# Kernel optimization log

Hardware: AMD Instinct MI355X
Metric: run time of the kernel (lower is better)

Reference implementation:

```python
import jax, jax.numpy as jnp
import numpy as np

M, K, N = 4096, 4096, 4096          # tokens, in_features, out_features
ROW_BLOCK, COL_BLOCK = 1, 4          # sparse block shape (rows x cols of W)
BLOCK_DENSITY = 0.2                  # fraction of nonzero blocks


def setup_inputs() -> dict:
    key = jax.random.key(0)
    k1, k2, k3, k4 = jax.random.split(key, 4)
    # quint8 activations stored as int32 in [0, 255]
    x_q = jax.random.randint(k1, (M, K), 0, 256, dtype=jnp.int32)
    # qint8 weights stored as int32 in [-127, 127], zero_point == 0
    w_dense = jax.random.randint(k2, (N, K), -127, 128, dtype=jnp.int32)
    # block-sparse structure: zero out whole ROW_BLOCK x COL_BLOCK blocks
    blk_mask = jax.random.bernoulli(k3, BLOCK_DENSITY, (N // ROW_BLOCK, K // COL_BLOCK))
    mask = jnp.repeat(jnp.repeat(blk_mask, ROW_BLOCK, axis=0), COL_BLOCK, axis=1)
    w_q = jnp.where(mask, w_dense, 0)
    bias = jax.random.normal(k4, (N,), dtype=jnp.float32) * 0.1
    return dict(
        x_q=x_q,
        w_q=w_q,
        bias=bias,
        x_scale=jnp.float32(0.05),
        x_zp=jnp.int32(128),
        w_scale=jnp.float32(0.01),
        out_scale=jnp.float32(0.1),
        out_zp=jnp.int32(128),
    )


def reference(x_q, w_q, bias, x_scale, x_zp, w_scale, out_scale, out_zp):
    # int32 accumulate of (x - x_zp) @ W^T over the (block-)sparse weight
    acc = jnp.einsum('mk,nk->mn', x_q - x_zp, w_q)  # [M, N] int32
    # dequantize + bias
    y = acc.astype(jnp.float32) * (x_scale * w_scale) + bias[None, :]
    # requantize to quint8 (stored as int32)
    q = jnp.round(y / out_scale).astype(jnp.int32) + out_zp
    return jnp.clip(q, 0, 255)
```

## Files before the change

### kernel.cpp

```cpp
#include <hip/hip_runtime.h>
#include <stdint.h>

#define MDIM 4096
#define NDIM 4096
#define KDIM 4096
#define BM 128
#define BN 128
#define BKB 128

typedef int i32x4 __attribute__((ext_vector_type(4)));

typedef __attribute__((address_space(1))) const void gv_t;
typedef __attribute__((address_space(3))) void lv_t;

__device__ __forceinline__ int pack4(int a, int b, int c, int d) {
    return (a & 0xFF) | ((b & 0xFF) << 8) | ((c & 0xFF) << 16) | ((d & 0xFF) << 24);
}

__global__ void pack_x_kernel(const int* __restrict__ x, const int* __restrict__ zp_p,
                              int* __restrict__ out, int total16) {
    const int zp = zp_p[0];
    int idx = blockIdx.x * blockDim.x + threadIdx.x;
    int stride = gridDim.x * blockDim.x;
    for (int i = idx; i < total16; i += stride) {
        const int4* src = (const int4*)(x + (long)i * 16);
        int4 a = src[0], b = src[1], c = src[2], d = src[3];
        int4 r;
        r.x = pack4(a.x - zp, a.y - zp, a.z - zp, a.w - zp);
        r.y = pack4(b.x - zp, b.y - zp, b.z - zp, b.w - zp);
        r.z = pack4(c.x - zp, c.y - zp, c.z - zp, c.w - zp);
        r.w = pack4(d.x - zp, d.y - zp, d.z - zp, d.w - zp);
        ((int4*)out)[i] = r;
    }
}

__global__ void pack_w_kernel(const int* __restrict__ w, int* __restrict__ out, int total16) {
    int idx = blockIdx.x * blockDim.x + threadIdx.x;
    int stride = gridDim.x * blockDim.x;
    for (int i = idx; i < total16; i += stride) {
        const int4* src = (const int4*)(w + (long)i * 16);
        int4 a = src[0], b = src[1], c = src[2], d = src[3];
        int4 r;
        r.x = pack4(a.x, a.y, a.z, a.w);
        r.y = pack4(b.x, b.y, b.z, b.w);
        r.z = pack4(c.x, c.y, c.z, c.w);
        r.w = pack4(d.x, d.y, d.z, d.w);
        ((int4*)out)[i] = r;
    }
}

__global__ __launch_bounds__(256)
void gemm_i8_kernel(const char* __restrict__ A8, const char* __restrict__ B8,
                    const float* __restrict__ bias,
                    const float* __restrict__ xs_p, const float* __restrict__ ws_p,
                    const float* __restrict__ os_p, const int* __restrict__ ozp_p,
                    int* __restrict__ out) {
    __shared__ char lsA[BM * BKB];
    __shared__ char lsB[BN * BKB];

    const int t = threadIdx.x;
    const int lane = t & 63;
    const int wave = t >> 6;
    const int wr = wave >> 1;
    const int wc = wave & 1;
    const long brow = (long)blockIdx.y * BM;
    const long bcol = (long)blockIdx.x * BN;

    i32x4 acc[4][4] = {};

    int st_row[4], st_off[4];
    #pragma unroll
    for (int i = 0; i < 4; ++i) {
        int c = t + i * 256;
        int r = c >> 3, s = c & 7;
        st_row[i] = r;
        st_off[i] = (s ^ (r & 7)) * 16;
    }

    for (int kt = 0; kt < KDIM; kt += BKB) {
        #pragma unroll
        for (int i = 0; i < 4; ++i) {
            int c16 = (t + i * 256) * 16;
            __builtin_amdgcn_global_load_lds(
                (gv_t*)(A8 + (brow + st_row[i]) * KDIM + kt + st_off[i]),
                (lv_t*)(lsA + c16), 16, 0, 0);
            __builtin_amdgcn_global_load_lds(
                (gv_t*)(B8 + (bcol + st_row[i]) * KDIM + kt + st_off[i]),
                (lv_t*)(lsB + c16), 16, 0, 0);
        }
        __syncthreads();

        i32x4 af[4][2], bf[4][2];
        #pragma unroll
        for (int mi = 0; mi < 4; ++mi) {
            int row = wr * 64 + mi * 16 + (lane & 15);
            #pragma unroll
            for (int kk = 0; kk < 2; ++kk) {
                int ls = kk * 4 + (lane >> 4);
                af[mi][kk] = *(const i32x4*)(lsA + row * BKB + ((ls ^ (row & 7)) * 16));
            }
        }
        #pragma unroll
        for (int ni = 0; ni < 4; ++ni) {
            int row = wc * 64 + ni * 16 + (lane & 15);
            #pragma unroll
            for (int kk = 0; kk < 2; ++kk) {
                int ls = kk * 4 + (lane >> 4);
                bf[ni][kk] = *(const i32x4*)(lsB + row * BKB + ((ls ^ (row & 7)) * 16));
            }
        }

        #pragma unroll
        for (int mi = 0; mi < 4; ++mi)
            #pragma unroll
            for (int ni = 0; ni < 4; ++ni) {
                acc[mi][ni] = __builtin_amdgcn_mfma_i32_16x16x64_i8(af[mi][0], bf[ni][0], acc[mi][ni], 0, 0, 0);
                acc[mi][ni] = __builtin_amdgcn_mfma_i32_16x16x64_i8(af[mi][1], bf[ni][1], acc[mi][ni], 0, 0, 0);
            }
        __syncthreads();
    }

    const float scale = xs_p[0] * ws_p[0];
    const float os = os_p[0];
    const int ozp = ozp_p[0];
    #pragma unroll
    for (int mi = 0; mi < 4; ++mi) {
        long row0 = brow + wr * 64 + mi * 16 + (lane >> 4) * 4;
        #pragma unroll
        for (int ni = 0; ni < 4; ++ni) {
            long col = bcol + wc * 64 + ni * 16 + (lane & 15);
            float bv = bias[col];
            #pragma unroll
            for (int r = 0; r < 4; ++r) {
                float y = (float)acc[mi][ni][r] * scale + bv;
                int q = (int)rintf(y / os) + ozp;
                q = q < 0 ? 0 : (q > 255 ? 255 : q);
                out[(row0 + r) * NDIM + col] = q;
            }
        }
    }
}

__global__ void naive_gemm_kernel(const int* __restrict__ x, const int* __restrict__ w,
                                  const float* __restrict__ bias,
                                  const float* __restrict__ xs_p, const int* __restrict__ xzp_p,
                                  const float* __restrict__ ws_p, const float* __restrict__ os_p,
                                  const int* __restrict__ ozp_p, int* __restrict__ out) {
    long idx = (long)blockIdx.x * blockDim.x + threadIdx.x;
    if (idx >= (long)MDIM * NDIM) return;
    int m = idx >> 12, n = idx & (NDIM - 1);
    const int4* xr = (const int4*)(x + (long)m * KDIM);
    const int4* wv = (const int4*)(w + (long)n * KDIM);
    const int zp = xzp_p[0];
    int acc = 0;
    for (int k = 0; k < KDIM / 4; ++k) {
        int4 a = xr[k], b = wv[k];
        acc += (a.x - zp) * b.x + (a.y - zp) * b.y + (a.z - zp) * b.z + (a.w - zp) * b.w;
    }
    float y = (float)acc * (xs_p[0] * ws_p[0]) + bias[n];
    int q = (int)rintf(y / os_p[0]) + ozp_p[0];
    out[idx] = q < 0 ? 0 : (q > 255 ? 255 : q);
}

extern "C" void kernel_launch(void* const* d_in, const int* in_sizes, int n_in,
                              void* d_out, int out_size, void* d_ws, size_t ws_size,
                              hipStream_t stream) {
    const int*   x_q  = (const int*)d_in[0];
    const int*   w_q  = (const int*)d_in[1];
    const float* bias = (const float*)d_in[2];
    const float* xs   = (const float*)d_in[3];
    const int*   xzp  = (const int*)d_in[4];
    const float* wsc  = (const float*)d_in[5];
    const float* osc  = (const float*)d_in[6];
    const int*   ozp  = (const int*)d_in[7];
    int* out = (int*)d_out;

    const size_t need = 2UL * MDIM * KDIM;
    if (ws_size >= need) {
        char* A8 = (char*)d_ws;
        char* B8 = A8 + (size_t)MDIM * KDIM;
        const int total16 = MDIM * KDIM / 16;
        pack_x_kernel<<<2048, 256, 0, stream>>>(x_q, xzp, (int*)A8, total16);
        pack_w_kernel<<<2048, 256, 0, stream>>>(w_q, (int*)B8, total16);
        dim3 grid(NDIM / BN, MDIM / BM);
        gemm_i8_kernel<<<grid, 256, 0, stream>>>(A8, B8, bias, xs, wsc, osc, ozp, out);
    } else {
        long total = (long)MDIM * NDIM;
        naive_gemm_kernel<<<(total + 255) / 256, 256, 0, stream>>>(
            x_q, w_q, bias, xs, xzp, wsc, osc, ozp, out);
    }
}
```

Baseline: 262.3 us.

## Rewrite int8 GEMM as 256x256 tile, double-buffered, eight-phase pipelined kernel

Grows the GEMM tile to 256x256 with 512 threads. It double-buffers LDS at 128KB and interleaves the global-to-LDS staging of the next tiles with four MFMA sub-phases, using explicit waitcnt, barriers and setprio. It also swizzles the workgroup order for L2 locality and simplifies the pack kernels to one int4 per thread. The aim is to hide global load latency and raise MFMA utilisation, at the cost of heavier register and LDS use, a grid of only 256 workgroups, and more barriers.

```diff
diff --git a/kernel.cpp b/kernel.cpp
--- a/kernel.cpp
+++ b/kernel.cpp
@@ -4,100 +4,100 @@
 #define MDIM 4096
 #define NDIM 4096
 #define KDIM 4096
-#define BM 128
-#define BN 128
+#define BM 256
+#define BN 256
 #define BKB 128
+#define NT (KDIM / BKB)
 
 typedef int i32x4 __attribute__((ext_vector_type(4)));
 
 typedef __attribute__((address_space(1))) const void gv_t;
 typedef __attribute__((address_space(3))) void lv_t;
 
+#define BAR() do { asm volatile("" ::: "memory"); __builtin_amdgcn_s_barrier(); asm volatile("" ::: "memory"); } while (0)
+
 __device__ __forceinline__ int pack4(int a, int b, int c, int d) {
     return (a & 0xFF) | ((b & 0xFF) << 8) | ((c & 0xFF) << 16) | ((d & 0xFF) << 24);
 }
 
 __global__ void pack_x_kernel(const int* __restrict__ x, const int* __restrict__ zp_p,
-                              int* __restrict__ out, int total16) {
+                              int* __restrict__ out, int total4) {
     const int zp = zp_p[0];
-    int idx = blockIdx.x * blockDim.x + threadIdx.x;
-    int stride = gridDim.x * blockDim.x;
-    for (int i = idx; i < total16; i += stride) {
-        const int4* src = (const int4*)(x + (long)i * 16);
-        int4 a = src[0], b = src[1], c = src[2], d = src[3];
-        int4 r;
-        r.x = pack4(a.x - zp, a.y - zp, a.z - zp, a.w - zp);
-        r.y = pack4(b.x - zp, b.y - zp, b.z - zp, b.w - zp);
-        r.z = pack4(c.x - zp, c.y - zp, c.z - zp, c.w - zp);
-        r.w = pack4(d.x - zp, d.y - zp, d.z - zp, d.w - zp);
-        ((int4*)out)[i] = r;
-    }
-}
-
-__global__ void pack_w_kernel(const int* __restrict__ w, int* __restrict__ out, int total16) {
-    int idx = blockIdx.x * blockDim.x + threadIdx.x;
-    int stride = gridDim.x * blockDim.x;
-    for (int i = idx; i < total16; i += stride) {
-        const int4* src = (const int4*)(w + (long)i * 16);
-        int4 a = src[0], b = src[1], c = src[2], d = src[3];
-        int4 r;
-        r.x = pack4(a.x, a.y, a.z, a.w);
-        r.y = pack4(b.x, b.y, b.z, b.w);
-        r.z = pack4(c.x, c.y, c.z, c.w);
-        r.w = pack4(d.x, d.y, d.z, d.w);
-        ((int4*)out)[i] = r;
-    }
-}
-
-__global__ __launch_bounds__(256)
-void gemm_i8_kernel(const char* __restrict__ A8, const char* __restrict__ B8,
-                    const float* __restrict__ bias,
-                    const float* __restrict__ xs_p, const float* __restrict__ ws_p,
-                    const float* __restrict__ os_p, const int* __restrict__ ozp_p,
-                    int* __restrict__ out) {
-    __shared__ char lsA[BM * BKB];
-    __shared__ char lsB[BN * BKB];
+    int i = blockIdx.x * blockDim.x + threadIdx.x;
+    if (i < total4) {
+        int4 a = ((const int4*)x)[i];
+        out[i] = pack4(a.x - zp, a.y - zp, a.z - zp, a.w - zp);
+    }
+}
+
+__global__ void pack_w_kernel(const int* __restrict__ w, int* __restrict__ out, int total4) {
+    int i = blockIdx.x * blockDim.x + threadIdx.x;
+    if (i < total4) {
+        int4 a = ((const int4*)w)[i];
+        out[i] = pack4(a.x, a.y, a.z, a.w);
+    }
+}
+
+__global__ __launch_bounds__(512, 2)
+void gemm_i8_8ph(const char* __restrict__ A8, const char* __restrict__ B8,
+                 const float* __restrict__ bias,
+                 const float* __restrict__ xs_p, const float* __restrict__ ws_p,
+                 const float* __restrict__ os_p, const int* __restrict__ ozp_p,
+                 int* __restrict__ out) {
+    __shared__ char lds[131072];
 
     const int t = threadIdx.x;
     const int lane = t & 63;
     const int wave = t >> 6;
-    const int wr = wave >> 1;
-    const int wc = wave & 1;
-    const long brow = (long)blockIdx.y * BM;
-    const long bcol = (long)blockIdx.x * BN;
-
-    i32x4 acc[4][4] = {};
-
-    int st_row[4], st_off[4];
-    #pragma unroll
-    for (int i = 0; i < 4; ++i) {
-        int c = t + i * 256;
-        int r = c >> 3, s = c & 7;
-        st_row[i] = r;
-        st_off[i] = (s ^ (r & 7)) * 16;
-    }
-
-    for (int kt = 0; kt < KDIM; kt += BKB) {
-        #pragma unroll
-        for (int i = 0; i < 4; ++i) {
-            int c16 = (t + i * 256) * 16;
+    const int wr = wave >> 2;
+    const int wc = wave & 3;
+
+    int wg = blockIdx.x;
+    int swz = (wg & 7) * (256 / 8) + (wg >> 3);
+    const long brow = (long)(swz >> 4) * BM;
+    const long bcol = (long)(swz & 15) * BN;
+
+    i32x4 acc[8][4] = {};
+
+    auto STAGE_HALF = [&](int tt, int h) {
+        if (tt >= NT) return;
+        const int d = tt & 1;
+        const char* src = (h < 2) ? A8 : B8;
+        const long base_rc = (h < 2) ? brow : bcol;
+        const int rh = h & 1;
+        const int kt = tt * BKB;
+        char* ldsbase = lds + ((h < 2) ? 0 : 65536) + d * 32768;
+        #pragma unroll
+        for (int j = 0; j < 2; ++j) {
+            int chunk = rh * 1024 + t + j * 512;
+            int row = chunk >> 3, slot = chunk & 7;
             __builtin_amdgcn_global_load_lds(
-                (gv_t*)(A8 + (brow + st_row[i]) * KDIM + kt + st_off[i]),
-                (lv_t*)(lsA + c16), 16, 0, 0);
-            __builtin_amdgcn_global_load_lds(
-                (gv_t*)(B8 + (bcol + st_row[i]) * KDIM + kt + st_off[i]),
-                (lv_t*)(lsB + c16), 16, 0, 0);
-        }
-        __syncthreads();
-
-        i32x4 af[4][2], bf[4][2];
-        #pragma unroll
-        for (int mi = 0; mi < 4; ++mi) {
-            int row = wr * 64 + mi * 16 + (lane & 15);
+                (gv_t*)(src + (base_rc + row) * KDIM + kt + ((slot ^ (row & 7)) * 16)),
+                (lv_t*)(ldsbase + chunk * 16), 16, 0, 0);
+        }
+    };
+
+    STAGE_HALF(0, 0); STAGE_HALF(0, 1); STAGE_HALF(0, 2); STAGE_HALF(0, 3);
+    STAGE_HALF(1, 0); STAGE_HALF(1, 1); STAGE_HALF(1, 2);
+
+    for (int tt = 0; tt < NT; ++tt) {
+        const int d = tt & 1;
+        const char* Ac = lds + d * 32768;
+        const char* Bc = lds + 65536 + d * 32768;
+
+        STAGE_HALF(tt + 1, 3);
+        if (tt == NT - 1) asm volatile("s_waitcnt vmcnt(0)" ::: "memory");
+        else              asm volatile("s_waitcnt vmcnt(8)" ::: "memory");
+        BAR();
+
+        i32x4 af[8][2], bf[4][2];
+        #pragma unroll
+        for (int mi = 0; mi < 8; ++mi) {
+            int row = wr * 128 + mi * 16 + (lane & 15);
             #pragma unroll
             for (int kk = 0; kk < 2; ++kk) {
                 int ls = kk * 4 + (lane >> 4);
-                af[mi][kk] = *(const i32x4*)(lsA + row * BKB + ((ls ^ (row & 7)) * 16));
+                af[mi][kk] = *(const i32x4*)(Ac + row * BKB + ((ls ^ (row & 7)) * 16));
             }
         }
         #pragma unroll
@@ -106,26 +106,68 @@
             #pragma unroll
             for (int kk = 0; kk < 2; ++kk) {
                 int ls = kk * 4 + (lane >> 4);
-                bf[ni][kk] = *(const i32x4*)(lsB + row * BKB + ((ls ^ (row & 7)) * 16));
+                bf[ni][kk] = *(const i32x4*)(Bc + row * BKB + ((ls ^ (row & 7)) * 16));
             }
         }
 
+        __builtin_amdgcn_s_setprio(1);
         #pragma unroll
         for (int mi = 0; mi < 4; ++mi)
             #pragma unroll
-            for (int ni = 0; ni < 4; ++ni) {
-                acc[mi][ni] = __builtin_amdgcn_mfma_i32_16x16x64_i8(af[mi][0], bf[ni][0], acc[mi][ni], 0, 0, 0);
-                acc[mi][ni] = __builtin_amdgcn_mfma_i32_16x16x64_i8(af[mi][1], bf[ni][1], acc[mi][ni], 0, 0, 0);
-            }
-        __syncthreads();
+            for (int ni = 0; ni < 2; ++ni)
+                #pragma unroll
+                for (int kk = 0; kk < 2; ++kk)
+                    acc[mi][ni] = __builtin_amdgcn_mfma_i32_16x16x64_i8(af[mi][kk], bf[ni][kk], acc[mi][ni], 0, 0, 0);
+        __builtin_amdgcn_s_setprio(0);
+        asm volatile("s_waitcnt lgkmcnt(0)" ::: "memory");
+        BAR();
+
+        STAGE_HALF(tt + 2, 0);
+        BAR();
+        __builtin_amdgcn_s_setprio(1);
+        #pragma unroll
+        for (int mi = 0; mi < 4; ++mi)
+            #pragma unroll
+            for (int ni = 2; ni < 4; ++ni)
+                #pragma unroll
+                for (int kk = 0; kk < 2; ++kk)
+                    acc[mi][ni] = __builtin_amdgcn_mfma_i32_16x16x64_i8(af[mi][kk], bf[ni][kk], acc[mi][ni], 0, 0, 0);
+        __builtin_amdgcn_s_setprio(0);
+        BAR();
+
+        STAGE_HALF(tt + 2, 1);
+        BAR();
+        __builtin_amdgcn_s_setprio(1);
+        #pragma unroll
+        for (int mi = 4; mi < 8; ++mi)
+            #pragma unroll
+            for (int ni = 0; ni < 2; ++ni)
+                #pragma unroll
+                for (int kk = 0; kk < 2; ++kk)
+                    acc[mi][ni] = __builtin_amdgcn_mfma_i32_16x16x64_i8(af[mi][kk], bf[ni][kk], acc[mi][ni], 0, 0, 0);
+        __builtin_amdgcn_s_setprio(0);
+        BAR();
+
+        STAGE_HALF(tt + 2, 2);
+        BAR();
+        __builtin_amdgcn_s_setprio(1);
+        #pragma unroll
+        for (int mi = 4; mi < 8; ++mi)
+            #pragma unroll
+            for (int ni = 2; ni < 4; ++ni)
+                #pragma unroll
+                for (int kk = 0; kk < 2; ++kk)
+                    acc[mi][ni] = __builtin_amdgcn_mfma_i32_16x16x64_i8(af[mi][kk], bf[ni][kk], acc[mi][ni], 0, 0, 0);
+        __builtin_amdgcn_s_setprio(0);
+        BAR();
     }
 
     const float scale = xs_p[0] * ws_p[0];
     const float os = os_p[0];
     const int ozp = ozp_p[0];
     #pragma unroll
-    for (int mi = 0; mi < 4; ++mi) {
-        long row0 = brow + wr * 64 + mi * 16 + (lane >> 4) * 4;
+    for (int mi = 0; mi < 8; ++mi) {
+        long row0 = brow + wr * 128 + mi * 16 + (lane >> 4) * 4;
         #pragma unroll
         for (int ni = 0; ni < 4; ++ni) {
             long col = bcol + wc * 64 + ni * 16 + (lane & 15);
@@ -179,11 +221,11 @@
     if (ws_size >= need) {
         char* A8 = (char*)d_ws;
         char* B8 = A8 + (size_t)MDIM * KDIM;
-        const int total16 = MDIM * KDIM / 16;
-        pack_x_kernel<<<2048, 256, 0, stream>>>(x_q, xzp, (int*)A8, total16);
-        pack_w_kernel<<<2048, 256, 0, stream>>>(w_q, (int*)B8, total16);
-        dim3 grid(NDIM / BN, MDIM / BM);
-        gemm_i8_kernel<<<grid, 256, 0, stream>>>(A8, B8, bias, xs, wsc, osc, ozp, out);
+        const int total4 = MDIM * KDIM / 4;
+        pack_x_kernel<<<total4 / 256, 256, 0, stream>>>(x_q, xzp, (int*)A8, total4);
+        pack_w_kernel<<<total4 / 256, 256, 0, stream>>>(w_q, (int*)B8, total4);
+        gemm_i8_8ph<<<(MDIM / BM) * (NDIM / BN), 512, 0, stream>>>(
+            A8, B8, bias, xs, wsc, osc, ozp, out);
     } else {
         long total = (long)MDIM * NDIM;
         naive_gemm_kernel<<<(total + 255) / 256, 256, 0, stream>>>(
```

Measured after the change: 236.4 us. -9.9%, faster.
